# Kernel tuning notes

Hardware: AMD Instinct MI355X
Metric: run time of the kernel (lower is better)

## Reference

```python
import jax, jax.numpy as jnp
import numpy as np

N_INPUT = 32
N_NEURONS = 64
N_OUTPUT = 16
BATCH = 2_000_000


def setup_inputs() -> dict:
    key = jax.random.key(0)
    k_in, k0, k1, k2 = jax.random.split(key, 4)
    inputs = jax.random.normal(k_in, (BATCH, N_INPUT), dtype=jnp.float32)
    # torch.nn.Linear(in, out, bias=False) weights have shape [out, in],
    # init U(-1/sqrt(in), 1/sqrt(in)).
    def init_w(k, fan_in, fan_out):
        b = 1.0 / np.sqrt(fan_in)
        return jax.random.uniform(k, (fan_out, fan_in), dtype=jnp.float32,
                                  minval=-b, maxval=b)
    W0 = init_w(k0, N_INPUT, N_NEURONS)     # [64, 32]
    W1 = init_w(k1, N_NEURONS, N_NEURONS)   # [64, 64]
    W2 = init_w(k2, N_NEURONS, N_OUTPUT)    # [16, 64]
    return {"inputs": inputs, "W0": W0, "W1": W1, "W2": W2}


def reference(inputs, W0, W1, W2):
    # x @ W.T for each bias-free layer, ReLU between all but the last.
    x = jax.nn.relu(jnp.einsum('bi,ni->bn', inputs, W0))
    x = jax.nn.relu(jnp.einsum('bn,mn->bm', x, W1))
    x = jnp.einsum('bm,om->bo', x, W2)
    return x
```

## Files before the change

### kernel.cpp

```cpp
#include <hip/hip_runtime.h>
#include <hip/hip_bf16.h>

typedef float f32x4 __attribute__((ext_vector_type(4)));
typedef _Float16 f16x8 __attribute__((ext_vector_type(8)));
typedef _Float16 f16x4 __attribute__((ext_vector_type(4)));

#define WAVES 4
#define COLSTR 36

__device__ __forceinline__ f32x4 mfma16(f16x8 a, f16x8 b, f32x4 c) {
    return __builtin_amdgcn_mfma_f32_16x16x32_f16(a, b, c, 0, 0, 0);
}

__device__ __forceinline__ f16x8 cvt8(f32x4 a, f32x4 b) {
    f16x8 h;
#pragma unroll
    for (int j = 0; j < 4; ++j) { h[j] = (_Float16)a[j]; h[j + 4] = (_Float16)b[j]; }
    return h;
}

__device__ __forceinline__ f16x4 relu_pk(f32x4 a) {
    f16x4 v;
#pragma unroll
    for (int j = 0; j < 4; ++j) v[j] = (_Float16)fmaxf(a[j], 0.0f);
    return v;
}

__global__ __launch_bounds__(256, 3) void mlp_kernel(
    const float* __restrict__ X, const float* __restrict__ W0,
    const float* __restrict__ W1, const float* __restrict__ W2,
    float* __restrict__ Y, int ntiles)
{
    __shared__ float ldsA[WAVES][2][16 * COLSTR];
    __shared__ float ldsB[WAVES][2][16 * COLSTR];
    const int tid  = threadIdx.x;
    const int wid  = tid >> 6;
    const int lane = tid & 63;
    const int b16  = lane & 15;
    const int g    = lane >> 4;

    f16x8 w0[4], w1[4][2], w2[2];
#pragma unroll
    for (int t = 0; t < 4; ++t) {
        const float* p = W0 + (16 * t + b16) * 32 + 8 * g;
        w0[t] = cvt8(*(const f32x4*)p, *(const f32x4*)(p + 4));
    }
#pragma unroll
    for (int t = 0; t < 4; ++t) {
#pragma unroll
        for (int s = 0; s < 2; ++s) {
            const float* p = W1 + (16 * t + b16) * 64 + 32 * s + 8 * g;
            w1[t][s] = cvt8(*(const f32x4*)p, *(const f32x4*)(p + 4));
        }
    }
#pragma unroll
    for (int s = 0; s < 2; ++s) {
        const float* p = W2 + b16 * 64 + 32 * s + 8 * g;
        w2[s] = cvt8(*(const f32x4*)p, *(const f32x4*)(p + 4));
    }

    const int xoff  = b16 * 32 + 8 * g;
    const int yoff  = b16 * 16 + 4 * g;
    const int wbase = COLSTR * b16 + 2 * g;
    const int rbase = COLSTR * b16 + 4 * g;

    float* A0 = &ldsA[wid][0][0];
    float* A1 = &ldsA[wid][1][0];
    float* B0 = &ldsB[wid][0][0];
    float* B1 = &ldsB[wid][1][0];

    const int npairs = (ntiles + 1) >> 1;
    const int gwid = blockIdx.x * WAVES + wid;
    const int gstr = gridDim.x * WAVES;
    if (gwid >= npairs) return;

    int pair = gwid;
    {
    }
    const float* xp = X + (size_t)(2 * pair) * 512 + xoff;
    size_t off1 = (2 * pair + 1 < ntiles) ? 512 : 0;
    f32x4 x00 = *(const f32x4*)xp;
    f32x4 x01 = *(const f32x4*)(xp + 4);
    f32x4 x10 = *(const f32x4*)(xp + off1);
    f32x4 x11 = *(const f32x4*)(xp + off1 + 4);

    while (true) {
        const int next = pair + gstr;
        const bool have_next = next < npairs;
        const int pf = have_next ? next : pair;
        const float* np = X + (size_t)(2 * pf) * 512 + xoff;
        const size_t noff1 = (2 * pf + 1 < ntiles) ? 512 : 0;
        f32x4 n00 = *(const f32x4*)np;
        f32x4 n01 = *(const f32x4*)(np + 4);
        f32x4 n10 = *(const f32x4*)(np + noff1);
        f32x4 n11 = *(const f32x4*)(np + noff1 + 4);

        f16x8 xa = cvt8(x00, x01);
        f16x8 xb = cvt8(x10, x11);
        f32x4 acc0[4], acc1[4];
#pragma unroll
        for (int t = 0; t < 4; ++t) {
            f32x4 z = {0.f, 0.f, 0.f, 0.f};
            acc0[t] = mfma16(w0[t], xa, z);
            acc1[t] = mfma16(w0[t], xb, z);
        }
#pragma unroll
        for (int t = 0; t < 4; ++t) {
            *(f16x4*)(A0 + wbase + 8 * t) = relu_pk(acc0[t]);
            *(f16x4*)(A1 + wbase + 8 * t) = relu_pk(acc1[t]);
        }

        f32x4 c0[4], c1[4];
#pragma unroll
        for (int t = 0; t < 4; ++t) {
            c0[t] = (f32x4){0.f, 0.f, 0.f, 0.f};
            c1[t] = (f32x4){0.f, 0.f, 0.f, 0.f};
        }
#pragma unroll
        for (int s = 0; s < 2; ++s) {
            f16x8 p0 = *(const f16x8*)(A0 + rbase + 16 * s);
            f16x8 p1 = *(const f16x8*)(A1 + rbase + 16 * s);
#pragma unroll
            for (int t = 0; t < 4; ++t) {
                c0[t] = mfma16(w1[t][s], p0, c0[t]);
                c1[t] = mfma16(w1[t][s], p1, c1[t]);
            }
        }
#pragma unroll
        for (int t = 0; t < 4; ++t) {
            *(f16x4*)(B0 + wbase + 8 * t) = relu_pk(c0[t]);
            *(f16x4*)(B1 + wbase + 8 * t) = relu_pk(c1[t]);
        }

        f32x4 o0 = {0.f, 0.f, 0.f, 0.f};
        f32x4 o1 = {0.f, 0.f, 0.f, 0.f};
#pragma unroll
        for (int s = 0; s < 2; ++s) {
            f16x8 q0 = *(const f16x8*)(B0 + rbase + 16 * s);
            f16x8 q1 = *(const f16x8*)(B1 + rbase + 16 * s);
            o0 = mfma16(w2[s], q0, o0);
            o1 = mfma16(w2[s], q1, o1);
        }
        float* yp = Y + (size_t)(2 * pair) * 256 + yoff;
        *(f32x4*)yp = o0;
        *(f32x4*)(yp + (off1 ? 256 : 0)) = o1;

        if (!have_next) break;
        pair = next;
        off1 = noff1;
        x00 = n00; x01 = n01; x10 = n10; x11 = n11;
    }
}

extern "C" void kernel_launch(void* const* d_in, const int* in_sizes, int n_in,
                              void* d_out, int out_size, void* d_ws, size_t ws_size,
                              hipStream_t stream) {
    const float* X  = (const float*)d_in[0];
    const float* W0 = (const float*)d_in[1];
    const float* W1 = (const float*)d_in[2];
    const float* W2 = (const float*)d_in[3];
    float* Y = (float*)d_out;

    const int batch  = in_sizes[0] / 32;
    const int ntiles = batch / 16;
    const int npairs = (ntiles + 1) >> 1;

    int blocks = 768;
    if (blocks * WAVES > npairs) blocks = (npairs + WAVES - 1) / WAVES;

    hipLaunchKernelGGL(mlp_kernel, dim3(blocks), dim3(256), 0, stream,
                       X, W0, W1, W2, Y, ntiles);
}
```

Before: 82.75 us.

## Keep MLP activations in registers by permuting weight K layout, drop LDS

The layer-1 and layer-2 weight fragments are loaded with a permuted K ordering so that the packed relu outputs of one MFMA can feed the next MFMA's B operand directly from registers. This removes every LDS write and read of intermediate activations between layers. Occupancy is raised to 4 blocks per CU and the grid grows to 1024 blocks. Register pressure rises, and the two tiles are now processed sequentially, which may reduce MFMA interleaving.

```diff
diff --git a/kernel.cpp b/kernel.cpp
--- a/kernel.cpp
+++ b/kernel.cpp
@@ -1,12 +1,12 @@
 #include <hip/hip_runtime.h>
-#include <hip/hip_bf16.h>
 
 typedef float f32x4 __attribute__((ext_vector_type(4)));
 typedef _Float16 f16x8 __attribute__((ext_vector_type(8)));
 typedef _Float16 f16x4 __attribute__((ext_vector_type(4)));
+typedef int i32x4 __attribute__((ext_vector_type(4)));
+typedef int i32x2 __attribute__((ext_vector_type(2)));
 
 #define WAVES 4
-#define COLSTR 36
 
 __device__ __forceinline__ f32x4 mfma16(f16x8 a, f16x8 b, f32x4 c) {
     return __builtin_amdgcn_mfma_f32_16x16x32_f16(a, b, c, 0, 0, 0);
@@ -19,20 +19,23 @@
     return h;
 }
 
-__device__ __forceinline__ f16x4 relu_pk(f32x4 a) {
+__device__ __forceinline__ i32x2 relu_pk2(f32x4 a) {
     f16x4 v;
 #pragma unroll
     for (int j = 0; j < 4; ++j) v[j] = (_Float16)fmaxf(a[j], 0.0f);
-    return v;
+    return __builtin_bit_cast(i32x2, v);
 }
 
-__global__ __launch_bounds__(256, 3) void mlp_kernel(
+__device__ __forceinline__ f16x8 cat(i32x2 a, i32x2 b) {
+    i32x4 v; v[0] = a[0]; v[1] = a[1]; v[2] = b[0]; v[3] = b[1];
+    return __builtin_bit_cast(f16x8, v);
+}
+
+__global__ __launch_bounds__(256, 4) void mlp_kernel(
     const float* __restrict__ X, const float* __restrict__ W0,
     const float* __restrict__ W1, const float* __restrict__ W2,
     float* __restrict__ Y, int ntiles)
 {
-    __shared__ float ldsA[WAVES][2][16 * COLSTR];
-    __shared__ float ldsB[WAVES][2][16 * COLSTR];
     const int tid  = threadIdx.x;
     const int wid  = tid >> 6;
     const int lane = tid & 63;
@@ -49,25 +52,18 @@
     for (int t = 0; t < 4; ++t) {
 #pragma unroll
         for (int s = 0; s < 2; ++s) {
-            const float* p = W1 + (16 * t + b16) * 64 + 32 * s + 8 * g;
-            w1[t][s] = cvt8(*(const f32x4*)p, *(const f32x4*)(p + 4));
+            const float* p = W1 + (16 * t + b16) * 64 + 32 * s + 4 * g;
+            w1[t][s] = cvt8(*(const f32x4*)p, *(const f32x4*)(p + 16));
         }
     }
 #pragma unroll
     for (int s = 0; s < 2; ++s) {
-        const float* p = W2 + b16 * 64 + 32 * s + 8 * g;
-        w2[s] = cvt8(*(const f32x4*)p, *(const f32x4*)(p + 4));
+        const float* p = W2 + b16 * 64 + 32 * s + 4 * g;
+        w2[s] = cvt8(*(const f32x4*)p, *(const f32x4*)(p + 16));
     }
 
-    const int xoff  = b16 * 32 + 8 * g;
-    const int yoff  = b16 * 16 + 4 * g;
-    const int wbase = COLSTR * b16 + 2 * g;
-    const int rbase = COLSTR * b16 + 4 * g;
-
-    float* A0 = &ldsA[wid][0][0];
-    float* A1 = &ldsA[wid][1][0];
-    float* B0 = &ldsB[wid][0][0];
-    float* B1 = &ldsB[wid][1][0];
+    const int xoff = b16 * 32 + 8 * g;
+    const int yoff = b16 * 16 + 4 * g;
 
     const int npairs = (ntiles + 1) >> 1;
     const int gwid = blockIdx.x * WAVES + wid;
@@ -75,14 +71,10 @@
     if (gwid >= npairs) return;
 
     int pair = gwid;
-    {
-    }
     const float* xp = X + (size_t)(2 * pair) * 512 + xoff;
     size_t off1 = (2 * pair + 1 < ntiles) ? 512 : 0;
-    f32x4 x00 = *(const f32x4*)xp;
-    f32x4 x01 = *(const f32x4*)(xp + 4);
-    f32x4 x10 = *(const f32x4*)(xp + off1);
-    f32x4 x11 = *(const f32x4*)(xp + off1 + 4);
+    f32x4 x00 = *(const f32x4*)xp;          f32x4 x01 = *(const f32x4*)(xp + 4);
+    f32x4 x10 = *(const f32x4*)(xp + off1); f32x4 x11 = *(const f32x4*)(xp + off1 + 4);
 
     while (true) {
         const int next = pair + gstr;
@@ -90,60 +82,44 @@
         const int pf = have_next ? next : pair;
         const float* np = X + (size_t)(2 * pf) * 512 + xoff;
         const size_t noff1 = (2 * pf + 1 < ntiles) ? 512 : 0;
-        f32x4 n00 = *(const f32x4*)np;
-        f32x4 n01 = *(const f32x4*)(np + 4);
-        f32x4 n10 = *(const f32x4*)(np + noff1);
-        f32x4 n11 = *(const f32x4*)(np + noff1 + 4);
+        f32x4 n00 = *(const f32x4*)np;           f32x4 n01 = *(const f32x4*)(np + 4);
+        f32x4 n10 = *(const f32x4*)(np + noff1); f32x4 n11 = *(const f32x4*)(np + noff1 + 4);
 
-        f16x8 xa = cvt8(x00, x01);
-        f16x8 xb = cvt8(x10, x11);
-        f32x4 acc0[4], acc1[4];
+        i32x2 pk[2][4];
 #pragma unroll
-        for (int t = 0; t < 4; ++t) {
-            f32x4 z = {0.f, 0.f, 0.f, 0.f};
-            acc0[t] = mfma16(w0[t], xa, z);
-            acc1[t] = mfma16(w0[t], xb, z);
-        }
+        for (int u = 0; u < 2; ++u) {
+            f16x8 xa = cvt8(u ? x10 : x00, u ? x11 : x01);
 #pragma unroll
-        for (int t = 0; t < 4; ++t) {
-            *(f16x4*)(A0 + wbase + 8 * t) = relu_pk(acc0[t]);
-            *(f16x4*)(A1 + wbase + 8 * t) = relu_pk(acc1[t]);
+            for (int t = 0; t < 4; ++t) {
+                f32x4 z = {0.f, 0.f, 0.f, 0.f};
+                z = mfma16(w0[t], xa, z);
+                pk[u][t] = relu_pk2(z);
+            }
         }
 
-        f32x4 c0[4], c1[4];
 #pragma unroll
-        for (int t = 0; t < 4; ++t) {
-            c0[t] = (f32x4){0.f, 0.f, 0.f, 0.f};
-            c1[t] = (f32x4){0.f, 0.f, 0.f, 0.f};
+        for (int u = 0; u < 2; ++u) {
+            f32x4 c[4];
+#pragma unroll
+            for (int t = 0; t < 4; ++t) c[t] = (f32x4){0.f, 0.f, 0.f, 0.f};
+            const f16x8 f0 = cat(pk[u][0], pk[u][1]);
+#pragma unroll
+            for (int t = 0; t < 4; ++t) c[t] = mfma16(w1[t][0], f0, c[t]);
+            const f16x8 f1 = cat(pk[u][2], pk[u][3]);
+#pragma unroll
+            for (int t = 0; t < 4; ++t) c[t] = mfma16(w1[t][1], f1, c[t]);
+
+            i32x2 q[4];
+#pragma unroll
+            for (int t = 0; t < 4; ++t) q[t] = relu_pk2(c[t]);
+
+            f32x4 o = {0.f, 0.f, 0.f, 0.f};
+            o = mfma16(w2[0], cat(q[0], q[1]), o);
+            o = mfma16(w2[1], cat(q[2], q[3]), o);
+
+            float* yp = Y + (size_t)(2 * pair) * 256 + yoff;
+            *(f32x4*)(yp + (u ? (off1 ? 256 : 0) : 0)) = o;
         }
-#pragma unroll
-        for (int s = 0; s < 2; ++s) {
-            f16x8 p0 = *(const f16x8*)(A0 + rbase + 16 * s);
-            f16x8 p1 = *(const f16x8*)(A1 + rbase + 16 * s);
-#pragma unroll
-            for (int t = 0; t < 4; ++t) {
-                c0[t] = mfma16(w1[t][s], p0, c0[t]);
-                c1[t] = mfma16(w1[t][s], p1, c1[t]);
-            }
-        }
-#pragma unroll
-        for (int t = 0; t < 4; ++t) {
-            *(f16x4*)(B0 + wbase + 8 * t) = relu_pk(c0[t]);
-            *(f16x4*)(B1 + wbase + 8 * t) = relu_pk(c1[t]);
-        }
-
-        f32x4 o0 = {0.f, 0.f, 0.f, 0.f};
-        f32x4 o1 = {0.f, 0.f, 0.f, 0.f};
-#pragma unroll
-        for (int s = 0; s < 2; ++s) {
-            f16x8 q0 = *(const f16x8*)(B0 + rbase + 16 * s);
-            f16x8 q1 = *(const f16x8*)(B1 + rbase + 16 * s);
-            o0 = mfma16(w2[s], q0, o0);
-            o1 = mfma16(w2[s], q1, o1);
-        }
-        float* yp = Y + (size_t)(2 * pair) * 256 + yoff;
-        *(f32x4*)yp = o0;
-        *(f32x4*)(yp + (off1 ? 256 : 0)) = o1;
 
         if (!have_next) break;
         pair = next;
@@ -165,7 +141,7 @@
     const int ntiles = batch / 16;
     const int npairs = (ntiles + 1) >> 1;
 
-    int blocks = 768;
+    int blocks = 1024;
     if (blocks * WAVES > npairs) blocks = (npairs + WAVES - 1) / WAVES;
 
     hipLaunchKernelGGL(mlp_kernel, dim3(blocks), dim3(256), 0, stream,
```

Measured after the change: 85.88 us. +3.8%, slower.
